# Performance work log

Measured on AMD Instinct MI355X. Metric: run time of the kernel, lower is better.

The kernel has to match this reference:

```python
import jax, jax.numpy as jnp
import numpy as np

B, T, I, H, L = 64, 2048, 128, 128, 2  # batch, seq_len, input, hidden, layers


def setup_inputs() -> dict:
    key = jax.random.key(0)
    ks = jax.random.split(key, 6)
    w = lambda k, shape: jax.random.normal(k, shape, dtype=jnp.float32) * 0.05
    return {
        "x": jax.random.normal(ks[0], (B, T, I), dtype=jnp.float32),
        "Wx0": w(ks[1], (4 * H, I)),
        "Wh0": w(ks[2], (4 * H, H)),
        "b0": jnp.zeros((4 * H,), jnp.float32),
        "Wx1": w(ks[3], (4 * H, H)),
        "Wh1": w(ks[4], (4 * H, H)),
        "b1": jnp.zeros((4 * H,), jnp.float32),
    }


def _cell(x_t, h, c, Wx, Wh, b):
    # fused-gate GEMM; gate order (i, f, g, o) matches the torch cell exactly
    gates = x_t @ Wx.T + h @ Wh.T + b  # [B, 4H]
    i, f, g, o = jnp.split(gates, 4, axis=-1)
    i = jax.nn.sigmoid(i)
    f = jax.nn.sigmoid(f)
    g = jnp.tanh(g)
    o = jax.nn.sigmoid(o)
    c_new = f * c + i * g
    h_new = o * jnp.tanh(c_new)
    return h_new, c_new


def reference(x, Wx0, Wh0, b0, Wx1, Wh1, b1):
    params = [(Wx0, Wh0, b0), (Wx1, Wh1, b1)]
    bsz = x.shape[0]
    hidden = Wh0.shape[1]
    h0 = jnp.zeros((L, bsz, hidden), x.dtype)
    c0 = jnp.zeros((L, bsz, hidden), x.dtype)

    def step(carry, x_t):
        h, c = carry
        hs, cs = [], []
        inp = x_t
        for l, (Wx, Wh, b) in enumerate(params):  # fixed, tiny layer loop
            hl, cl = _cell(inp, h[l], c[l], Wx, Wh, b)
            inp = hl
            hs.append(hl)
            cs.append(cl)
        return (jnp.stack(hs), jnp.stack(cs)), inp

    (hT, cT), ys = jax.lax.scan(step, (h0, c0), jnp.swapaxes(x, 0, 1))
    output = jnp.swapaxes(ys, 0, 1)  # [B, T, H], top-layer hidden states
    return output, hT, cT
```

## Files before the change

kernel.cpp:

```cpp
#include <hip/hip_runtime.h>
#include <hip/hip_fp16.h>

#define BB 64
#define TT 2048
#define II 128
#define HH 128
#define NG 512
#define CH 128
#define NCH (TT / CH)

typedef _Float16 h2_t __attribute__((ext_vector_type(2)));

#if defined(__has_builtin)
#if __has_builtin(__builtin_amdgcn_fdot2)
#define HAVE_FDOT2 1
#endif
#endif

__device__ __forceinline__ float fdot2f(h2_t a, h2_t b, float c) {
#ifdef HAVE_FDOT2
  return __builtin_amdgcn_fdot2(a, b, c, false);
#else
  return c + (float)a[0] * (float)b[0] + (float)a[1] * (float)b[1];
#endif
}

__device__ __forceinline__ float fast_sigmoid(float x) {
  float t = __builtin_amdgcn_exp2f(-1.4426950408889634f * x);
  return __builtin_amdgcn_rcpf(1.0f + t);
}
__device__ __forceinline__ float act_gate(float x, bool tanh_sel) {
  float xx = tanh_sel ? 2.0f * x : x;
  float s = fast_sigmoid(xx);
  return tanh_sel ? 2.0f * s - 1.0f : s;
}
__device__ __forceinline__ float fast_tanh(float x) {
  return 2.0f * fast_sigmoid(2.0f * x) - 1.0f;
}

__device__ __forceinline__ float dpp_xor1(float x) {
  return __int_as_float(__builtin_amdgcn_update_dpp(0, __float_as_int(x), 0xB1, 0xF, 0xF, true));
}
__device__ __forceinline__ float dpp_xor2(float x) {
  return __int_as_float(__builtin_amdgcn_update_dpp(0, __float_as_int(x), 0x4E, 0xF, 0xF, true));
}

__device__ __forceinline__ void bar_lds() {
  __builtin_amdgcn_fence(__ATOMIC_RELEASE, "workgroup", "local");
  __builtin_amdgcn_s_barrier();
  __builtin_amdgcn_fence(__ATOMIC_ACQUIRE, "workgroup", "local");
}

union LD4 {
  float4 f4;
  h2_t h[4];
};
union LDB {
  uint4 u4;
  h2_t h[4];
};

__device__ __forceinline__ unsigned aload(unsigned* p) { return atomicAdd(p, 0u); }

__global__ void w_transpose(const float* __restrict__ W, float* __restrict__ WT) {
  int idx = blockIdx.x * 256 + threadIdx.x;
  if (idx < NG * II) {
    int n = idx >> 7;
    int k = idx & 127;
    WT[k * NG + n] = W[idx];
  }
}

__global__ __launch_bounds__(256) void xg_gemm(const float* __restrict__ X,
                                               const float* __restrict__ WT,
                                               const float* __restrict__ bias,
                                               __half* __restrict__ Xg) {
  __shared__ float As[64][132];
  __shared__ float Bs[128][64];
  const int m0 = blockIdx.x * 64;
  const int n0 = blockIdx.y * 64;
  const int tid = threadIdx.x;

  {
    const float4* xv = (const float4*)(X + (size_t)m0 * II);
#pragma unroll
    for (int r = 0; r < 8; ++r) {
      int f = tid + 256 * r;
      int m = f >> 5;
      int c4 = f & 31;
      float4 v = xv[m * 32 + c4];
      *(float4*)&As[m][c4 * 4] = v;
    }
  }
  {
#pragma unroll
    for (int r = 0; r < 8; ++r) {
      int f = tid + 256 * r;
      int k = f >> 4;
      int q = f & 15;
      float4 v = *(const float4*)(WT + (size_t)k * NG + n0 + q * 4);
      *(float4*)&Bs[k][q * 4] = v;
    }
  }
  __syncthreads();

  const int tx = tid & 15;
  const int ty = tid >> 4;
  float acc[4][4];
#pragma unroll
  for (int i = 0; i < 4; ++i)
#pragma unroll
    for (int j = 0; j < 4; ++j) acc[i][j] = 0.0f;

#pragma unroll 4
  for (int k = 0; k < 128; ++k) {
    float a0 = As[ty * 4 + 0][k];
    float a1 = As[ty * 4 + 1][k];
    float a2 = As[ty * 4 + 2][k];
    float a3 = As[ty * 4 + 3][k];
    float4 bv = *(const float4*)&Bs[k][tx * 4];
    acc[0][0] = fmaf(a0, bv.x, acc[0][0]);
    acc[0][1] = fmaf(a0, bv.y, acc[0][1]);
    acc[0][2] = fmaf(a0, bv.z, acc[0][2]);
    acc[0][3] = fmaf(a0, bv.w, acc[0][3]);
    acc[1][0] = fmaf(a1, bv.x, acc[1][0]);
    acc[1][1] = fmaf(a1, bv.y, acc[1][1]);
    acc[1][2] = fmaf(a1, bv.z, acc[1][2]);
    acc[1][3] = fmaf(a1, bv.w, acc[1][3]);
    acc[2][0] = fmaf(a2, bv.x, acc[2][0]);
    acc[2][1] = fmaf(a2, bv.y, acc[2][1]);
    acc[2][2] = fmaf(a2, bv.z, acc[2][2]);
    acc[2][3] = fmaf(a2, bv.w, acc[2][3]);
    acc[3][0] = fmaf(a3, bv.x, acc[3][0]);
    acc[3][1] = fmaf(a3, bv.y, acc[3][1]);
    acc[3][2] = fmaf(a3, bv.z, acc[3][2]);
    acc[3][3] = fmaf(a3, bv.w, acc[3][3]);
  }

  float4 bvec = *(const float4*)(bias + n0 + tx * 4);
#pragma unroll
  for (int i = 0; i < 4; ++i) {
    int m = m0 + ty * 4 + i;
    __half2* dst = (__half2*)(Xg + (size_t)m * NG + n0 + tx * 4);
    dst[0] = __halves2half2(__float2half(acc[i][0] + bvec.x),
                            __float2half(acc[i][1] + bvec.y));
    dst[1] = __halves2half2(__float2half(acc[i][2] + bvec.z),
                            __float2half(acc[i][3] + bvec.w));
  }
}


__device__ __forceinline__ void roleA(int b, int n, char* smem,
    const __half* Xg, const float* __restrict__ Wh0,
    float* __restrict__ out, __half* hstream, unsigned* flag0)
{
  const int j = n >> 2;
  const int p = n & 3;
  const bool tsel = (p == 2);

  h2_t wh[4][16];
#pragma unroll
  for (int g = 0; g < 4; ++g) {
    const float2* ph = (const float2*)(Wh0 + (size_t)(g * 128 + j) * HH + p * 32);
#pragma unroll
    for (int k = 0; k < 16; ++k) {
      float2 v = ph[k];
      wh[g][k][0] = (_Float16)v.x;
      wh[g][k][1] = (_Float16)v.y;
    }
  }

  _Float16(*hb)[HH] = (_Float16(*)[HH])smem;
  if (n < HH) {
    hb[0][n] = (_Float16)0.0f;
    hb[1][n] = (_Float16)0.0f;
  }
  float c = 0.0f, hv = 0.0f;
  __syncthreads();

  const __half* xs = Xg + (size_t)b * TT * NG + p * 128 + j;
  float* hT = out + (size_t)BB * TT * HH;
  float* cT = hT + 2 * BB * HH;
  __half* hsp = hstream + (size_t)b * TT * HH + j;

  __half xg_c = xs[0];

#pragma unroll 1
  for (int cc = 0; cc < NCH; ++cc) {
#pragma unroll 1
    for (int s = 0; s < CH; ++s) {
      const int i = cc * CH + s;
      const int ip = (i + 1 < TT) ? i + 1 : i;
      __half xg_n = xs[(size_t)ip * NG];

      const char* H = (const char*)hb[i & 1] + p * 64;
      float a0 = 0.f, a1 = 0.f, a2 = 0.f, a3 = 0.f;
#pragma unroll
      for (int q = 0; q < 4; ++q) {
        LD4 u;
        u.f4 = *(const float4*)(H + q * 16);
#pragma unroll
        for (int t = 0; t < 4; ++t) {
          const int m = q * 4 + t;
          a0 = fdot2f(wh[0][m], u.h[t], a0);
          a1 = fdot2f(wh[1][m], u.h[t], a1);
          a2 = fdot2f(wh[2][m], u.h[t], a2);
          a3 = fdot2f(wh[3][m], u.h[t], a3);
        }
      }
      float k01 = (p & 1) ? a1 : a0;
      float u01 = (p & 1) ? a0 : a1;
      float r01 = k01 + dpp_xor1(u01);
      float k23 = (p & 1) ? a3 : a2;
      float u23 = (p & 1) ? a2 : a3;
      float r23 = k23 + dpp_xor1(u23);
      float kA = (p & 2) ? r23 : r01;
      float uA = (p & 2) ? r01 : r23;
      float sL = kA + dpp_xor2(uA);
      float aL = act_gate(sL + __half2float(xg_c), tsel);
      float fg = dpp_xor1(aL);
      float gg = dpp_xor2(aL);
      float og = dpp_xor2(fg);
      if (p == 0) {
        c = fg * c + aL * gg;
        hv = og * fast_tanh(c);
        _Float16 hf = (_Float16)hv;
        hb[(i & 1) ^ 1][j] = hf;
        *(_Float16*)(hsp + (size_t)i * HH) = hf;
      }
      bar_lds();
      xg_c = xg_n;
    }
    __syncthreads();
    if (n == 0) {
      __builtin_amdgcn_fence(__ATOMIC_RELEASE, "agent");
      atomicExch(flag0 + b * NCH + cc, 1u);
    }
  }

  if (p == 0) {
    hT[b * HH + j] = hv;
    cT[b * HH + j] = c;
  }
}

__device__ __forceinline__ void roleC(int cidx, int n, char* smem,
    __half* Xg, const __half* hstream, const float* __restrict__ WT1,
    const float* __restrict__ b1, unsigned* flag0, unsigned* flagC)
{
  const int b = cidx >> 1;
  const int half = cidx & 1;
  h2_t(*As2)[68] = (h2_t(*)[68])smem;
  h2_t(*Bs2)[64] = (h2_t(*)[64])(smem + 64 * 68 * 4);

  const int ty = n >> 4;
  const int tx = n & 15;

#pragma unroll 1
  for (int cc = 0; cc < NCH; ++cc) {
    if (n == 0) {
      while (aload(flag0 + b * NCH + cc) < 1u) __builtin_amdgcn_s_sleep(1);
    }
    __syncthreads();
    __builtin_amdgcn_fence(__ATOMIC_ACQUIRE, "agent");

    const int t0 = cc * CH + half * 64;
    {
      const int m = n >> 3, seg = n & 7;
      const uint4* src = (const uint4*)(hstream + ((size_t)b * TT + t0 + m) * HH + seg * 16);
      uint4 v0 = src[0], v1 = src[1];
      *(uint4*)&As2[m][seg * 8] = v0;
      *(uint4*)&As2[m][seg * 8 + 4] = v1;
    }

#pragma unroll 1
    for (int nt = 0; nt < 8; ++nt) {
      __syncthreads();
      {
        const int kp = n >> 3, cg = n & 7;
        const float4* w0 = (const float4*)(WT1 + (size_t)(2 * kp) * NG + nt * 64 + cg * 8);
        const float4* w1 = (const float4*)(WT1 + (size_t)(2 * kp + 1) * NG + nt * 64 + cg * 8);
        float4 x0 = w0[0], x1 = w0[1];
        float4 y0 = w1[0], y1 = w1[1];
        h2_t r[8];
        r[0][0] = (_Float16)x0.x; r[0][1] = (_Float16)y0.x;
        r[1][0] = (_Float16)x0.y; r[1][1] = (_Float16)y0.y;
        r[2][0] = (_Float16)x0.z; r[2][1] = (_Float16)y0.z;
        r[3][0] = (_Float16)x0.w; r[3][1] = (_Float16)y0.w;
        r[4][0] = (_Float16)x1.x; r[4][1] = (_Float16)y1.x;
        r[5][0] = (_Float16)x1.y; r[5][1] = (_Float16)y1.y;
        r[6][0] = (_Float16)x1.z; r[6][1] = (_Float16)y1.z;
        r[7][0] = (_Float16)x1.w; r[7][1] = (_Float16)y1.w;
        *(uint4*)&Bs2[kp][cg * 8] = *(uint4*)&r[0];
        *(uint4*)&Bs2[kp][cg * 8 + 4] = *(uint4*)&r[4];
      }
      __syncthreads();

      float acc[2][4];
#pragma unroll
      for (int r = 0; r < 2; ++r)
#pragma unroll
        for (int q = 0; q < 4; ++q) acc[r][q] = 0.0f;

#pragma unroll 4
      for (int k4 = 0; k4 < 16; ++k4) {
        LDB ua0, ua1;
        ua0.u4 = *(const uint4*)&As2[ty * 2][k4 * 4];
        ua1.u4 = *(const uint4*)&As2[ty * 2 + 1][k4 * 4];
#pragma unroll
        for (int t = 0; t < 4; ++t) {
          LDB ub;
          ub.u4 = *(const uint4*)&Bs2[k4 * 4 + t][tx * 4];
          acc[0][0] = fdot2f(ua0.h[t], ub.h[0], acc[0][0]);
          acc[0][1] = fdot2f(ua0.h[t], ub.h[1], acc[0][1]);
          acc[0][2] = fdot2f(ua0.h[t], ub.h[2], acc[0][2]);
          acc[0][3] = fdot2f(ua0.h[t], ub.h[3], acc[0][3]);
          acc[1][0] = fdot2f(ua1.h[t], ub.h[0], acc[1][0]);
          acc[1][1] = fdot2f(ua1.h[t], ub.h[1], acc[1][1]);
          acc[1][2] = fdot2f(ua1.h[t], ub.h[2], acc[1][2]);
          acc[1][3] = fdot2f(ua1.h[t], ub.h[3], acc[1][3]);
        }
      }

      const int col = nt * 64 + tx * 4;
      float4 bv = *(const float4*)(b1 + col);
#pragma unroll
      for (int r = 0; r < 2; ++r) {
        __half2* d = (__half2*)(Xg + ((size_t)b * TT + t0 + ty * 2 + r) * NG + col);
        d[0] = __halves2half2(__float2half(acc[r][0] + bv.x),
                              __float2half(acc[r][1] + bv.y));
        d[1] = __halves2half2(__float2half(acc[r][2] + bv.z),
                              __float2half(acc[r][3] + bv.w));
      }
    }
    __syncthreads();
    if (n == 0) {
      __builtin_amdgcn_fence(__ATOMIC_RELEASE, "agent");
      atomicAdd(flagC + b * NCH + cc, 1u);
    }
  }
}

__device__ __forceinline__ void roleB(int b, int n, char* smem,
    const __half* Xg, const float* __restrict__ Wh1,
    float* __restrict__ out, unsigned* flagC)
{
  const int j = n >> 2;
  const int p = n & 3;
  const bool tsel = (p == 2);

  h2_t wh[4][16];
#pragma unroll
  for (int g = 0; g < 4; ++g) {
    const float2* ph = (const float2*)(Wh1 + (size_t)(g * 128 + j) * HH + p * 32);
#pragma unroll
    for (int k = 0; k < 16; ++k) {
      float2 v = ph[k];
      wh[g][k][0] = (_Float16)v.x;
      wh[g][k][1] = (_Float16)v.y;
    }
  }

  _Float16(*hb)[HH] = (_Float16(*)[HH])smem;
  if (n < HH) {
    hb[0][n] = (_Float16)0.0f;
    hb[1][n] = (_Float16)0.0f;
  }
  float c = 0.0f, hv = 0.0f;
  __syncthreads();

  const __half* xs = Xg + (size_t)b * TT * NG + p * 128 + j;
  float* outp = out + (size_t)b * TT * HH;
  float* hT = out + (size_t)BB * TT * HH;
  float* cT = hT + 2 * BB * HH;

#pragma unroll 1
  for (int cc = 0; cc < NCH; ++cc) {
    if (n == 0) {
      while (aload(flagC + b * NCH + cc) < 2u) __builtin_amdgcn_s_sleep(1);
    }
    __syncthreads();
    __builtin_amdgcn_fence(__ATOMIC_ACQUIRE, "agent");

    __half xg_c = xs[(size_t)(cc * CH) * NG];
#pragma unroll 1
    for (int s = 0; s < CH; ++s) {
      const int i = cc * CH + s;
      __half xg_n = (s + 1 < CH) ? xs[(size_t)(i + 1) * NG] : __float2half(0.0f);

      const char* H = (const char*)hb[i & 1] + p * 64;
      float a0 = 0.f, a1 = 0.f, a2 = 0.f, a3 = 0.f;
#pragma unroll
      for (int q = 0; q < 4; ++q) {
        LD4 u;
        u.f4 = *(const float4*)(H + q * 16);
#pragma unroll
        for (int t = 0; t < 4; ++t) {
          const int m = q * 4 + t;
          a0 = fdot2f(wh[0][m], u.h[t], a0);
          a1 = fdot2f(wh[1][m], u.h[t], a1);
          a2 = fdot2f(wh[2][m], u.h[t], a2);
          a3 = fdot2f(wh[3][m], u.h[t], a3);
        }
      }
      float k01 = (p & 1) ? a1 : a0;
      float u01 = (p & 1) ? a0 : a1;
      float r01 = k01 + dpp_xor1(u01);
      float k23 = (p & 1) ? a3 : a2;
      float u23 = (p & 1) ? a2 : a3;
      float r23 = k23 + dpp_xor1(u23);
      float kA = (p & 2) ? r23 : r01;
      float uA = (p & 2) ? r01 : r23;
      float sL = kA + dpp_xor2(uA);
      float aL = act_gate(sL + __half2float(xg_c), tsel);
      float fg = dpp_xor1(aL);
      float gg = dpp_xor2(aL);
      float og = dpp_xor2(fg);
      if (p == 0) {
        c = fg * c + aL * gg;
        hv = og * fast_tanh(c);
        hb[(i & 1) ^ 1][j] = (_Float16)hv;
        outp[(size_t)i * HH + j] = hv;
      }
      bar_lds();
      xg_c = xg_n;
    }
  }

  if (p == 0) {
    hT[BB * HH + b * HH + j] = hv;
    cT[BB * HH + b * HH + j] = c;
  }
}

__global__
__attribute__((amdgpu_flat_work_group_size(512, 512)))
void lstm_mega(__half* Xg,
               __half* hstream,
               const float* __restrict__ Wh0,
               const float* __restrict__ Wh1,
               const float* __restrict__ WT1,
               const float* __restrict__ b1,
               float* __restrict__ out,
               unsigned* flag0, unsigned* flagC)
{
  __shared__ __align__(16) char smem[64 * 68 * 4 + 64 * 64 * 4];
  const int bid = blockIdx.x;
  const int n = threadIdx.x;
  if (bid < BB) {
    roleA(bid, n, smem, Xg, Wh0, out, hstream, flag0);
  } else if (bid < BB + 2 * BB) {
    roleC(bid - BB, n, smem, Xg, hstream, WT1, b1, flag0, flagC);
  } else {
    roleB(bid - 3 * BB, n, smem, Xg, Wh1, out, flagC);
  }
}

extern "C" void kernel_launch(void* const* d_in, const int* in_sizes, int n_in,
                              void* d_out, int out_size, void* d_ws, size_t ws_size,
                              hipStream_t stream) {
  const float* x   = (const float*)d_in[0];
  const float* Wx0 = (const float*)d_in[1];
  const float* Wh0 = (const float*)d_in[2];
  const float* b0  = (const float*)d_in[3];
  const float* Wx1 = (const float*)d_in[4];
  const float* Wh1 = (const float*)d_in[5];
  const float* b1  = (const float*)d_in[6];
  float* out = (float*)d_out;

  char* base = (char*)d_ws;
  __half* Xg = (__half*)base;
  size_t off = (size_t)BB * TT * NG * sizeof(__half);
  __half* hstream = (__half*)(base + off);
  off += (size_t)BB * TT * HH * sizeof(__half);
  float* WT0 = (float*)(base + off);
  off += (size_t)II * NG * sizeof(float);
  float* WT1 = (float*)(base + off);
  off += (size_t)II * NG * sizeof(float);
  unsigned* flag0 = (unsigned*)(base + off);
  off += (size_t)BB * NCH * sizeof(unsigned);
  unsigned* flagC = (unsigned*)(base + off);

  hipMemsetAsync(flag0, 0, 2 * (size_t)BB * NCH * sizeof(unsigned), stream);
  const int tgrid = (NG * II + 255) / 256;
  w_transpose<<<tgrid, 256, 0, stream>>>(Wx0, WT0);
  w_transpose<<<tgrid, 256, 0, stream>>>(Wx1, WT1);
  xg_gemm<<<dim3((BB * TT) / 64, NG / 64), 256, 0, stream>>>(x, WT0, b0, Xg);
  lstm_mega<<<4 * BB, 512, 0, stream>>>(Xg, hstream, Wh0, Wh1, WT1, b1, out,
                                        flag0, flagC);
}
```

Measured before the change: 1.538 ms.

## Batch 16 sequences per recurrent block and compute gates with MFMA

The recurrent roles for both layers are merged into one templated routine. Each workgroup now processes 16 batch rows at once and computes the hidden-to-gate product with 16x16x32 f16 MFMA instructions instead of per-sequence fdot2 plus DPP reductions. This cuts recurrent blocks from 64 per layer to 4, with the roleC flags aggregated per group of 16 sequences. The two weight transposes are fused into a single launch. The trade-off is far fewer workgroups on the serial path, with a per-step dependency on MFMA latency and a barrier.

```diff
diff --git a/kernel.cpp b/kernel.cpp
--- a/kernel.cpp
+++ b/kernel.cpp
@@ -8,8 +8,11 @@
 #define NG 512
 #define CH 128
 #define NCH (TT / CH)
+#define NA 4
 
 typedef _Float16 h2_t __attribute__((ext_vector_type(2)));
+typedef _Float16 f16x8 __attribute__((ext_vector_type(8)));
+typedef float f32x4 __attribute__((ext_vector_type(4)));
 
 #if defined(__has_builtin)
 #if __has_builtin(__builtin_amdgcn_fdot2)
@@ -29,20 +32,8 @@
   float t = __builtin_amdgcn_exp2f(-1.4426950408889634f * x);
   return __builtin_amdgcn_rcpf(1.0f + t);
 }
-__device__ __forceinline__ float act_gate(float x, bool tanh_sel) {
-  float xx = tanh_sel ? 2.0f * x : x;
-  float s = fast_sigmoid(xx);
-  return tanh_sel ? 2.0f * s - 1.0f : s;
-}
 __device__ __forceinline__ float fast_tanh(float x) {
   return 2.0f * fast_sigmoid(2.0f * x) - 1.0f;
-}
-
-__device__ __forceinline__ float dpp_xor1(float x) {
-  return __int_as_float(__builtin_amdgcn_update_dpp(0, __float_as_int(x), 0xB1, 0xF, 0xF, true));
-}
-__device__ __forceinline__ float dpp_xor2(float x) {
-  return __int_as_float(__builtin_amdgcn_update_dpp(0, __float_as_int(x), 0x4E, 0xF, 0xF, true));
 }
 
 __device__ __forceinline__ void bar_lds() {
@@ -51,24 +42,34 @@
   __builtin_amdgcn_fence(__ATOMIC_ACQUIRE, "workgroup", "local");
 }
 
-union LD4 {
+union LDH {
   float4 f4;
-  h2_t h[4];
+  f16x8 h8;
 };
 union LDB {
   uint4 u4;
   h2_t h[4];
 };
+union XU {
+  uint2 u;
+  __half h[4];
+};
+union HP {
+  _Float16 f[4];
+  uint2 u;
+};
 
 __device__ __forceinline__ unsigned aload(unsigned* p) { return atomicAdd(p, 0u); }
 
-__global__ void w_transpose(const float* __restrict__ W, float* __restrict__ WT) {
-  int idx = blockIdx.x * 256 + threadIdx.x;
-  if (idx < NG * II) {
-    int n = idx >> 7;
-    int k = idx & 127;
-    WT[k * NG + n] = W[idx];
-  }
+__global__ void w_transpose2(const float* __restrict__ W0, float* __restrict__ T0,
+                             const float* __restrict__ W1, float* __restrict__ T1) {
+  int bid = blockIdx.x;
+  const float* W = (bid < 256) ? W0 : W1;
+  float* T = (bid < 256) ? T0 : T1;
+  int idx = (bid & 255) * 256 + threadIdx.x;
+  int n = idx >> 7;
+  int k = idx & 127;
+  T[k * NG + n] = W[idx];
 }
 
 __global__ __launch_bounds__(256) void xg_gemm(const float* __restrict__ X,
@@ -149,104 +150,135 @@
   }
 }
 
-
-__device__ __forceinline__ void roleA(int b, int n, char* smem,
-    const __half* Xg, const float* __restrict__ Wh0,
-    float* __restrict__ out, __half* hstream, unsigned* flag0)
+#define HROW 136
+#define HBUF (16 * HROW)
+
+template <int LAYER>
+__device__ __forceinline__ void role_rec(int g, int tid, char* smem,
+    const __half* __restrict__ Xg, const float* __restrict__ Wh,
+    float* __restrict__ out, __half* __restrict__ hstream,
+    unsigned* flag0, unsigned* flagCg)
 {
-  const int j = n >> 2;
-  const int p = n & 3;
-  const bool tsel = (p == 2);
-
-  h2_t wh[4][16];
-#pragma unroll
-  for (int g = 0; g < 4; ++g) {
-    const float2* ph = (const float2*)(Wh0 + (size_t)(g * 128 + j) * HH + p * 32);
-#pragma unroll
-    for (int k = 0; k < 16; ++k) {
-      float2 v = ph[k];
-      wh[g][k][0] = (_Float16)v.x;
-      wh[g][k][1] = (_Float16)v.y;
-    }
-  }
-
-  _Float16(*hb)[HH] = (_Float16(*)[HH])smem;
-  if (n < HH) {
-    hb[0][n] = (_Float16)0.0f;
-    hb[1][n] = (_Float16)0.0f;
-  }
-  float c = 0.0f, hv = 0.0f;
+  const int w = tid >> 6;
+  const int l = tid & 63;
+  const int lrow = l & 15;
+  const int lk = l >> 4;
+  const int u0 = 16 * w + lk * 4;
+  const int bg = 16 * g + lrow;
+
+  f16x8 wf[4][4];
+#pragma unroll
+  for (int r = 0; r < 4; ++r)
+#pragma unroll
+    for (int kt = 0; kt < 4; ++kt) {
+      const float4* s4 = (const float4*)(Wh + (size_t)(128 * r + 16 * w + lrow) * HH + 32 * kt + 8 * lk);
+      float4 v0 = s4[0], v1 = s4[1];
+      f16x8 f;
+      f[0] = (_Float16)v0.x; f[1] = (_Float16)v0.y; f[2] = (_Float16)v0.z; f[3] = (_Float16)v0.w;
+      f[4] = (_Float16)v1.x; f[5] = (_Float16)v1.y; f[6] = (_Float16)v1.z; f[7] = (_Float16)v1.w;
+      wf[r][kt] = f;
+    }
+
+  _Float16* hb = (_Float16*)smem;
+  for (int i = tid; i < 2 * HBUF; i += 512) hb[i] = (_Float16)0.0f;
+  float c[4] = {0.f, 0.f, 0.f, 0.f};
+  float hq[4] = {0.f, 0.f, 0.f, 0.f};
   __syncthreads();
 
-  const __half* xs = Xg + (size_t)b * TT * NG + p * 128 + j;
+  const __half* XgL = Xg + (size_t)bg * TT * NG + u0;
   float* hT = out + (size_t)BB * TT * HH;
   float* cT = hT + 2 * BB * HH;
-  __half* hsp = hstream + (size_t)b * TT * HH + j;
-
-  __half xg_c = xs[0];
+  float* outp = out + (size_t)bg * TT * HH + u0;
+  __half* hsp = hstream + (size_t)bg * TT * HH + u0;
+
+  char* hbc = (char*)smem;
+  const int rdoff = lrow * (HROW * 2) + lk * 16;
+  const int wroff = lrow * (HROW * 2) + u0 * 2;
+
+  XU xc[4];
+  if (LAYER == 0) {
+#pragma unroll
+    for (int r = 0; r < 4; ++r) xc[r].u = *(const uint2*)(XgL + r * 128);
+  }
 
 #pragma unroll 1
   for (int cc = 0; cc < NCH; ++cc) {
+    if (LAYER == 1) {
+      if (tid == 0) {
+        while (aload(flagCg + g * NCH + cc) < 32u) __builtin_amdgcn_s_sleep(1);
+      }
+      __syncthreads();
+      __builtin_amdgcn_fence(__ATOMIC_ACQUIRE, "agent");
+      const __half* xb = XgL + (size_t)(cc * CH) * NG;
+#pragma unroll
+      for (int r = 0; r < 4; ++r) xc[r].u = *(const uint2*)(xb + r * 128);
+    }
+
 #pragma unroll 1
     for (int s = 0; s < CH; ++s) {
-      const int i = cc * CH + s;
-      const int ip = (i + 1 < TT) ? i + 1 : i;
-      __half xg_n = xs[(size_t)ip * NG];
-
-      const char* H = (const char*)hb[i & 1] + p * 64;
-      float a0 = 0.f, a1 = 0.f, a2 = 0.f, a3 = 0.f;
+      const int t = cc * CH + s;
+
+      const char* hr = hbc + (t & 1) * (HBUF * 2) + rdoff;
+      f32x4 a0 = {0.f, 0.f, 0.f, 0.f};
+      f32x4 a1 = a0, a2 = a0, a3 = a0;
+#pragma unroll
+      for (int kt = 0; kt < 4; ++kt) {
+        LDH u;
+        u.f4 = *(const float4*)(hr + kt * 64);
+        a0 = __builtin_amdgcn_mfma_f32_16x16x32_f16(wf[0][kt], u.h8, a0, 0, 0, 0);
+        a1 = __builtin_amdgcn_mfma_f32_16x16x32_f16(wf[1][kt], u.h8, a1, 0, 0, 0);
+        a2 = __builtin_amdgcn_mfma_f32_16x16x32_f16(wf[2][kt], u.h8, a2, 0, 0, 0);
+        a3 = __builtin_amdgcn_mfma_f32_16x16x32_f16(wf[3][kt], u.h8, a3, 0, 0, 0);
+      }
+
+      XU xn[4];
+      const bool pf = (LAYER == 0) ? (t + 1 < TT) : (s + 1 < CH);
+      if (pf) {
+        const __half* xb = XgL + (size_t)(t + 1) * NG;
+#pragma unroll
+        for (int r = 0; r < 4; ++r) xn[r].u = *(const uint2*)(xb + r * 128);
+      }
+
+      HP hp;
 #pragma unroll
       for (int q = 0; q < 4; ++q) {
-        LD4 u;
-        u.f4 = *(const float4*)(H + q * 16);
-#pragma unroll
-        for (int t = 0; t < 4; ++t) {
-          const int m = q * 4 + t;
-          a0 = fdot2f(wh[0][m], u.h[t], a0);
-          a1 = fdot2f(wh[1][m], u.h[t], a1);
-          a2 = fdot2f(wh[2][m], u.h[t], a2);
-          a3 = fdot2f(wh[3][m], u.h[t], a3);
-        }
-      }
-      float k01 = (p & 1) ? a1 : a0;
-      float u01 = (p & 1) ? a0 : a1;
-      float r01 = k01 + dpp_xor1(u01);
-      float k23 = (p & 1) ? a3 : a2;
-      float u23 = (p & 1) ? a2 : a3;
-      float r23 = k23 + dpp_xor1(u23);
-      float kA = (p & 2) ? r23 : r01;
-      float uA = (p & 2) ? r01 : r23;
-      float sL = kA + dpp_xor2(uA);
-      float aL = act_gate(sL + __half2float(xg_c), tsel);
-      float fg = dpp_xor1(aL);
-      float gg = dpp_xor2(aL);
-      float og = dpp_xor2(fg);
-      if (p == 0) {
-        c = fg * c + aL * gg;
-        hv = og * fast_tanh(c);
-        _Float16 hf = (_Float16)hv;
-        hb[(i & 1) ^ 1][j] = hf;
-        *(_Float16*)(hsp + (size_t)i * HH) = hf;
+        float gi = fast_sigmoid(a0[q] + __half2float(xc[0].h[q]));
+        float gf = fast_sigmoid(a1[q] + __half2float(xc[1].h[q]));
+        float gg = fast_tanh(a2[q] + __half2float(xc[2].h[q]));
+        float go = fast_sigmoid(a3[q] + __half2float(xc[3].h[q]));
+        c[q] = gf * c[q] + gi * gg;
+        float h = go * fast_tanh(c[q]);
+        hq[q] = h;
+        hp.f[q] = (_Float16)h;
+      }
+      *(uint2*)(hbc + ((t & 1) ^ 1) * (HBUF * 2) + wroff) = hp.u;
+      if (LAYER == 0) {
+        *(uint2*)(hsp + (size_t)t * HH) = hp.u;
+      } else {
+        float4 o4 = {hq[0], hq[1], hq[2], hq[3]};
+        *(float4*)(outp + (size_t)t * HH) = o4;
       }
       bar_lds();
-      xg_c = xg_n;
-    }
-    __syncthreads();
-    if (n == 0) {
+#pragma unroll
+      for (int r = 0; r < 4; ++r) xc[r].u = xn[r].u;
+    }
+
+    if (LAYER == 0) {
+      __syncthreads();
       __builtin_amdgcn_fence(__ATOMIC_RELEASE, "agent");
-      atomicExch(flag0 + b * NCH + cc, 1u);
-    }
-  }
-
-  if (p == 0) {
-    hT[b * HH + j] = hv;
-    cT[b * HH + j] = c;
-  }
+      if (tid < 16) atomicExch(flag0 + (16 * g + tid) * NCH + cc, 1u);
+    }
+  }
+
+  float4 hv4 = {hq[0], hq[1], hq[2], hq[3]};
+  float4 cv4 = {c[0], c[1], c[2], c[3]};
+  *(float4*)(hT + (size_t)LAYER * BB * HH + (size_t)bg * HH + u0) = hv4;
+  *(float4*)(cT + (size_t)LAYER * BB * HH + (size_t)bg * HH + u0) = cv4;
 }
 
 __device__ __forceinline__ void roleC(int cidx, int n, char* smem,
     __half* Xg, const __half* hstream, const float* __restrict__ WT1,
-    const float* __restrict__ b1, unsigned* flag0, unsigned* flagC)
+    const float* __restrict__ b1, unsigned* flag0, unsigned* flagCg)
 {
   const int b = cidx >> 1;
   const int half = cidx & 1;
@@ -336,123 +368,30 @@
     __syncthreads();
     if (n == 0) {
       __builtin_amdgcn_fence(__ATOMIC_RELEASE, "agent");
-      atomicAdd(flagC + b * NCH + cc, 1u);
-    }
-  }
-}
-
-__device__ __forceinline__ void roleB(int b, int n, char* smem,
-    const __half* Xg, const float* __restrict__ Wh1,
-    float* __restrict__ out, unsigned* flagC)
-{
-  const int j = n >> 2;
-  const int p = n & 3;
-  const bool tsel = (p == 2);
-
-  h2_t wh[4][16];
-#pragma unroll
-  for (int g = 0; g < 4; ++g) {
-    const float2* ph = (const float2*)(Wh1 + (size_t)(g * 128 + j) * HH + p * 32);
-#pragma unroll
-    for (int k = 0; k < 16; ++k) {
-      float2 v = ph[k];
-      wh[g][k][0] = (_Float16)v.x;
-      wh[g][k][1] = (_Float16)v.y;
-    }
-  }
-
-  _Float16(*hb)[HH] = (_Float16(*)[HH])smem;
-  if (n < HH) {
-    hb[0][n] = (_Float16)0.0f;
-    hb[1][n] = (_Float16)0.0f;
-  }
-  float c = 0.0f, hv = 0.0f;
-  __syncthreads();
-
-  const __half* xs = Xg + (size_t)b * TT * NG + p * 128 + j;
-  float* outp = out + (size_t)b * TT * HH;
-  float* hT = out + (size_t)BB * TT * HH;
-  float* cT = hT + 2 * BB * HH;
-
-#pragma unroll 1
-  for (int cc = 0; cc < NCH; ++cc) {
-    if (n == 0) {
-      while (aload(flagC + b * NCH + cc) < 2u) __builtin_amdgcn_s_sleep(1);
-    }
-    __syncthreads();
-    __builtin_amdgcn_fence(__ATOMIC_ACQUIRE, "agent");
-
-    __half xg_c = xs[(size_t)(cc * CH) * NG];
-#pragma unroll 1
-    for (int s = 0; s < CH; ++s) {
-      const int i = cc * CH + s;
-      __half xg_n = (s + 1 < CH) ? xs[(size_t)(i + 1) * NG] : __float2half(0.0f);
-
-      const char* H = (const char*)hb[i & 1] + p * 64;
-      float a0 = 0.f, a1 = 0.f, a2 = 0.f, a3 = 0.f;
-#pragma unroll
-      for (int q = 0; q < 4; ++q) {
-        LD4 u;
-        u.f4 = *(const float4*)(H + q * 16);
-#pragma unroll
-        for (int t = 0; t < 4; ++t) {
-          const int m = q * 4 + t;
-          a0 = fdot2f(wh[0][m], u.h[t], a0);
-          a1 = fdot2f(wh[1][m], u.h[t], a1);
-          a2 = fdot2f(wh[2][m], u.h[t], a2);
-          a3 = fdot2f(wh[3][m], u.h[t], a3);
-        }
-      }
-      float k01 = (p & 1) ? a1 : a0;
-      float u01 = (p & 1) ? a0 : a1;
-      float r01 = k01 + dpp_xor1(u01);
-      float k23 = (p & 1) ? a3 : a2;
-      float u23 = (p & 1) ? a2 : a3;
-      float r23 = k23 + dpp_xor1(u23);
-      float kA = (p & 2) ? r23 : r01;
-      float uA = (p & 2) ? r01 : r23;
-      float sL = kA + dpp_xor2(uA);
-      float aL = act_gate(sL + __half2float(xg_c), tsel);
-      float fg = dpp_xor1(aL);
-      float gg = dpp_xor2(aL);
-      float og = dpp_xor2(fg);
-      if (p == 0) {
-        c = fg * c + aL * gg;
-        hv = og * fast_tanh(c);
-        hb[(i & 1) ^ 1][j] = (_Float16)hv;
-        outp[(size_t)i * HH + j] = hv;
-      }
-      bar_lds();
-      xg_c = xg_n;
-    }
-  }
-
-  if (p == 0) {
-    hT[BB * HH + b * HH + j] = hv;
-    cT[BB * HH + b * HH + j] = c;
+      atomicAdd(flagCg + (b >> 4) * NCH + cc, 1u);
+    }
   }
 }
 
 __global__
 __attribute__((amdgpu_flat_work_group_size(512, 512)))
-void lstm_mega(__half* Xg,
-               __half* hstream,
+void lstm_mega(__half* Xg, __half* hstream,
                const float* __restrict__ Wh0,
                const float* __restrict__ Wh1,
                const float* __restrict__ WT1,
                const float* __restrict__ b1,
                float* __restrict__ out,
-               unsigned* flag0, unsigned* flagC)
+               unsigned* flag0, unsigned* flagCg)
 {
   __shared__ __align__(16) char smem[64 * 68 * 4 + 64 * 64 * 4];
   const int bid = blockIdx.x;
-  const int n = threadIdx.x;
-  if (bid < BB) {
-    roleA(bid, n, smem, Xg, Wh0, out, hstream, flag0);
-  } else if (bid < BB + 2 * BB) {
-    roleC(bid - BB, n, smem, Xg, hstream, WT1, b1, flag0, flagC);
+  const int tid = threadIdx.x;
+  if (bid < NA) {
+    role_rec<0>(bid, tid, smem, Xg, Wh0, out, hstream, flag0, flagCg);
+  } else if (bid < NA + 2 * BB) {
+    roleC(bid - NA, tid, smem, Xg, hstream, WT1, b1, flag0, flagCg);
   } else {
-    roleB(bid - 3 * BB, n, smem, Xg, Wh1, out, flagC);
+    role_rec<1>(bid - NA - 2 * BB, tid, smem, Xg, Wh1, out, hstream, flag0, flagCg);
   }
 }
 
@@ -478,14 +417,11 @@
   float* WT1 = (float*)(base + off);
   off += (size_t)II * NG * sizeof(float);
   unsigned* flag0 = (unsigned*)(base + off);
-  off += (size_t)BB * NCH * sizeof(unsigned);
-  unsigned* flagC = (unsigned*)(base + off);
-
-  hipMemsetAsync(flag0, 0, 2 * (size_t)BB * NCH * sizeof(unsigned), stream);
-  const int tgrid = (NG * II + 255) / 256;
-  w_transpose<<<tgrid, 256, 0, stream>>>(Wx0, WT0);
-  w_transpose<<<tgrid, 256, 0, stream>>>(Wx1, WT1);
+  unsigned* flagCg = flag0 + BB * NCH;
+
+  hipMemsetAsync(flag0, 0, (size_t)(BB * NCH + NA * NCH) * sizeof(unsigned), stream);
+  w_transpose2<<<512, 256, 0, stream>>>(Wx0, WT0, Wx1, WT1);
   xg_gemm<<<dim3((BB * TT) / 64, NG / 64), 256, 0, stream>>>(x, WT0, b0, Xg);
-  lstm_mega<<<4 * BB, 512, 0, stream>>>(Xg, hstream, Wh0, Wh1, WT1, b1, out,
-                                        flag0, flagC);
-}
+  lstm_mega<<<NA + 2 * BB + NA, 512, 0, stream>>>(Xg, hstream, Wh0, Wh1, WT1,
+                                                  b1, out, flag0, flagCg);
+}
```

Result: slower. 4.347 ms (+182.7%).

## Overlap layer-0 input projection with recurrence inside the persistent kernel

Applied to the files above, without the earlier changes.

The separate xg_gemm now computes only the first two time chunks (256 steps) per batch. The remaining chunks of the layer-0 input projection are computed by the roleC blocks two chunks ahead, which signal readiness through a new flagX counter that roleA waits on. The two weight-transpose launches are merged into one. The fdot2 accumulation chains in the recurrent roles are split into two partial sums to shorten dependency latency. This hides most of the large upfront GEMM behind the serial recurrence, at the cost of more spin-wait synchronisation and extra work on the roleC blocks.

```diff
diff --git a/kernel.cpp b/kernel.cpp
--- a/kernel.cpp
+++ b/kernel.cpp
@@ -62,27 +62,30 @@
 
 __device__ __forceinline__ unsigned aload(unsigned* p) { return atomicAdd(p, 0u); }
 
-__global__ void w_transpose(const float* __restrict__ W, float* __restrict__ WT) {
-  int idx = blockIdx.x * 256 + threadIdx.x;
-  if (idx < NG * II) {
-    int n = idx >> 7;
-    int k = idx & 127;
-    WT[k * NG + n] = W[idx];
-  }
-}
-
-__global__ __launch_bounds__(256) void xg_gemm(const float* __restrict__ X,
-                                               const float* __restrict__ WT,
-                                               const float* __restrict__ bias,
-                                               __half* __restrict__ Xg) {
+__global__ void w_transpose2(const float* __restrict__ W0, float* __restrict__ T0,
+                             const float* __restrict__ W1, float* __restrict__ T1) {
+  int bid = blockIdx.x;
+  const float* W = (bid < 256) ? W0 : W1;
+  float* T = (bid < 256) ? T0 : T1;
+  int idx = (bid & 255) * 256 + threadIdx.x;
+  int n = idx >> 7;
+  int k = idx & 127;
+  T[k * NG + n] = W[idx];
+}
+
+__global__ __launch_bounds__(256) void xg_gemm_pro(const float* __restrict__ X,
+                                                   const float* __restrict__ WT,
+                                                   const float* __restrict__ bias,
+                                                   __half* __restrict__ Xg) {
   __shared__ float As[64][132];
   __shared__ float Bs[128][64];
-  const int m0 = blockIdx.x * 64;
+  const int bx = blockIdx.x;
+  const size_t m0 = (size_t)(bx >> 2) * TT + (bx & 3) * 64;
   const int n0 = blockIdx.y * 64;
   const int tid = threadIdx.x;
 
   {
-    const float4* xv = (const float4*)(X + (size_t)m0 * II);
+    const float4* xv = (const float4*)(X + m0 * II);
 #pragma unroll
     for (int r = 0; r < 8; ++r) {
       int f = tid + 256 * r;
@@ -140,8 +143,8 @@
   float4 bvec = *(const float4*)(bias + n0 + tx * 4);
 #pragma unroll
   for (int i = 0; i < 4; ++i) {
-    int m = m0 + ty * 4 + i;
-    __half2* dst = (__half2*)(Xg + (size_t)m * NG + n0 + tx * 4);
+    size_t m = m0 + ty * 4 + i;
+    __half2* dst = (__half2*)(Xg + m * NG + n0 + tx * 4);
     dst[0] = __halves2half2(__float2half(acc[i][0] + bvec.x),
                             __float2half(acc[i][1] + bvec.y));
     dst[1] = __halves2half2(__float2half(acc[i][2] + bvec.z),
@@ -152,7 +155,8 @@
 
 __device__ __forceinline__ void roleA(int b, int n, char* smem,
     const __half* Xg, const float* __restrict__ Wh0,
-    float* __restrict__ out, __half* hstream, unsigned* flag0)
+    float* __restrict__ out, __half* hstream,
+    unsigned* flag0, unsigned* flagX)
 {
   const int j = n >> 2;
   const int p = n & 3;
@@ -183,31 +187,49 @@
   float* cT = hT + 2 * BB * HH;
   __half* hsp = hstream + (size_t)b * TT * HH + j;
 
-  __half xg_c = xs[0];
-
 #pragma unroll 1
   for (int cc = 0; cc < NCH; ++cc) {
+    if (cc >= 2) {
+      if (n == 0) {
+        while (aload(flagX + b * NCH + cc) < 2u) __builtin_amdgcn_s_sleep(1);
+      }
+      __syncthreads();
+      __builtin_amdgcn_fence(__ATOMIC_ACQUIRE, "agent");
+    }
+    __half xg_c = xs[(size_t)(cc * CH) * NG];
+
 #pragma unroll 1
     for (int s = 0; s < CH; ++s) {
       const int i = cc * CH + s;
-      const int ip = (i + 1 < TT) ? i + 1 : i;
-      __half xg_n = xs[(size_t)ip * NG];
+      __half xg_n = (s + 1 < CH) ? xs[(size_t)(i + 1) * NG] : __float2half(0.0f);
 
       const char* H = (const char*)hb[i & 1] + p * 64;
-      float a0 = 0.f, a1 = 0.f, a2 = 0.f, a3 = 0.f;
+      float s0a = 0.f, s0b = 0.f, s1a = 0.f, s1b = 0.f;
+      float s2a = 0.f, s2b = 0.f, s3a = 0.f, s3b = 0.f;
 #pragma unroll
       for (int q = 0; q < 4; ++q) {
         LD4 u;
         u.f4 = *(const float4*)(H + q * 16);
-#pragma unroll
-        for (int t = 0; t < 4; ++t) {
-          const int m = q * 4 + t;
-          a0 = fdot2f(wh[0][m], u.h[t], a0);
-          a1 = fdot2f(wh[1][m], u.h[t], a1);
-          a2 = fdot2f(wh[2][m], u.h[t], a2);
-          a3 = fdot2f(wh[3][m], u.h[t], a3);
-        }
-      }
+        const int m = q * 4;
+        s0a = fdot2f(wh[0][m + 0], u.h[0], s0a);
+        s0b = fdot2f(wh[0][m + 2], u.h[2], s0b);
+        s1a = fdot2f(wh[1][m + 0], u.h[0], s1a);
+        s1b = fdot2f(wh[1][m + 2], u.h[2], s1b);
+        s2a = fdot2f(wh[2][m + 0], u.h[0], s2a);
+        s2b = fdot2f(wh[2][m + 2], u.h[2], s2b);
+        s3a = fdot2f(wh[3][m + 0], u.h[0], s3a);
+        s3b = fdot2f(wh[3][m + 2], u.h[2], s3b);
+        s0a = fdot2f(wh[0][m + 1], u.h[1], s0a);
+        s0b = fdot2f(wh[0][m + 3], u.h[3], s0b);
+        s1a = fdot2f(wh[1][m + 1], u.h[1], s1a);
+        s1b = fdot2f(wh[1][m + 3], u.h[3], s1b);
+        s2a = fdot2f(wh[2][m + 1], u.h[1], s2a);
+        s2b = fdot2f(wh[2][m + 3], u.h[3], s2b);
+        s3a = fdot2f(wh[3][m + 1], u.h[1], s3a);
+        s3b = fdot2f(wh[3][m + 3], u.h[3], s3b);
+      }
+      float a0 = s0a + s0b, a1 = s1a + s1b, a2 = s2a + s2b, a3 = s3a + s3b;
+
       float k01 = (p & 1) ? a1 : a0;
       float u01 = (p & 1) ? a0 : a1;
       float r01 = k01 + dpp_xor1(u01);
@@ -245,8 +267,10 @@
 }
 
 __device__ __forceinline__ void roleC(int cidx, int n, char* smem,
-    __half* Xg, const __half* hstream, const float* __restrict__ WT1,
-    const float* __restrict__ b1, unsigned* flag0, unsigned* flagC)
+    __half* Xg, const __half* hstream, const float* __restrict__ x,
+    const float* __restrict__ WT0, const float* __restrict__ b0,
+    const float* __restrict__ WT1, const float* __restrict__ b1,
+    unsigned* flag0, unsigned* flagC, unsigned* flagX)
 {
   const int b = cidx >> 1;
   const int half = cidx & 1;
@@ -255,9 +279,93 @@
 
   const int ty = n >> 4;
   const int tx = n & 15;
+  const int mf = n >> 3;
+  const int sf = n & 7;
 
 #pragma unroll 1
   for (int cc = 0; cc < NCH; ++cc) {
+    if (cc + 2 < NCH) {
+      const int t0x = (cc + 2) * CH + half * 64;
+      {
+        const float4* sx = (const float4*)(x + ((size_t)b * TT + t0x + mf) * II + sf * 16);
+        float4 p0 = sx[0], p1 = sx[1], p2 = sx[2], p3 = sx[3];
+        h2_t r[8];
+        r[0][0] = (_Float16)p0.x; r[0][1] = (_Float16)p0.y;
+        r[1][0] = (_Float16)p0.z; r[1][1] = (_Float16)p0.w;
+        r[2][0] = (_Float16)p1.x; r[2][1] = (_Float16)p1.y;
+        r[3][0] = (_Float16)p1.z; r[3][1] = (_Float16)p1.w;
+        r[4][0] = (_Float16)p2.x; r[4][1] = (_Float16)p2.y;
+        r[5][0] = (_Float16)p2.z; r[5][1] = (_Float16)p2.w;
+        r[6][0] = (_Float16)p3.x; r[6][1] = (_Float16)p3.y;
+        r[7][0] = (_Float16)p3.z; r[7][1] = (_Float16)p3.w;
+        *(uint4*)&As2[mf][sf * 8] = *(uint4*)&r[0];
+        *(uint4*)&As2[mf][sf * 8 + 4] = *(uint4*)&r[4];
+      }
+#pragma unroll 1
+      for (int nt = 0; nt < 8; ++nt) {
+        __syncthreads();
+        {
+          const int kp = n >> 3, cg = n & 7;
+          const float4* w0 = (const float4*)(WT0 + (size_t)(2 * kp) * NG + nt * 64 + cg * 8);
+          const float4* w1 = (const float4*)(WT0 + (size_t)(2 * kp + 1) * NG + nt * 64 + cg * 8);
+          float4 x0 = w0[0], x1 = w0[1];
+          float4 y0 = w1[0], y1 = w1[1];
+          h2_t r[8];
+          r[0][0] = (_Float16)x0.x; r[0][1] = (_Float16)y0.x;
+          r[1][0] = (_Float16)x0.y; r[1][1] = (_Float16)y0.y;
+          r[2][0] = (_Float16)x0.z; r[2][1] = (_Float16)y0.z;
+          r[3][0] = (_Float16)x0.w; r[3][1] = (_Float16)y0.w;
+          r[4][0] = (_Float16)x1.x; r[4][1] = (_Float16)y1.x;
+          r[5][0] = (_Float16)x1.y; r[5][1] = (_Float16)y1.y;
+          r[6][0] = (_Float16)x1.z; r[6][1] = (_Float16)y1.z;
+          r[7][0] = (_Float16)x1.w; r[7][1] = (_Float16)y1.w;
+          *(uint4*)&Bs2[kp][cg * 8] = *(uint4*)&r[0];
+          *(uint4*)&Bs2[kp][cg * 8 + 4] = *(uint4*)&r[4];
+        }
+        __syncthreads();
+
+        float acc[2][4];
+#pragma unroll
+        for (int r = 0; r < 2; ++r)
+#pragma unroll
+          for (int q = 0; q < 4; ++q) acc[r][q] = 0.0f;
+#pragma unroll 4
+        for (int k4 = 0; k4 < 16; ++k4) {
+          LDB ua0, ua1;
+          ua0.u4 = *(const uint4*)&As2[ty * 2][k4 * 4];
+          ua1.u4 = *(const uint4*)&As2[ty * 2 + 1][k4 * 4];
+#pragma unroll
+          for (int t = 0; t < 4; ++t) {
+            LDB ub;
+            ub.u4 = *(const uint4*)&Bs2[k4 * 4 + t][tx * 4];
+            acc[0][0] = fdot2f(ua0.h[t], ub.h[0], acc[0][0]);
+            acc[0][1] = fdot2f(ua0.h[t], ub.h[1], acc[0][1]);
+            acc[0][2] = fdot2f(ua0.h[t], ub.h[2], acc[0][2]);
+            acc[0][3] = fdot2f(ua0.h[t], ub.h[3], acc[0][3]);
+            acc[1][0] = fdot2f(ua1.h[t], ub.h[0], acc[1][0]);
+            acc[1][1] = fdot2f(ua1.h[t], ub.h[1], acc[1][1]);
+            acc[1][2] = fdot2f(ua1.h[t], ub.h[2], acc[1][2]);
+            acc[1][3] = fdot2f(ua1.h[t], ub.h[3], acc[1][3]);
+          }
+        }
+        const int col = nt * 64 + tx * 4;
+        float4 bv = *(const float4*)(b0 + col);
+#pragma unroll
+        for (int r = 0; r < 2; ++r) {
+          __half2* d = (__half2*)(Xg + ((size_t)b * TT + t0x + ty * 2 + r) * NG + col);
+          d[0] = __halves2half2(__float2half(acc[r][0] + bv.x),
+                                __float2half(acc[r][1] + bv.y));
+          d[1] = __halves2half2(__float2half(acc[r][2] + bv.z),
+                                __float2half(acc[r][3] + bv.w));
+        }
+      }
+      __syncthreads();
+      if (n == 0) {
+        __builtin_amdgcn_fence(__ATOMIC_RELEASE, "agent");
+        atomicAdd(flagX + b * NCH + cc + 2, 1u);
+      }
+    }
+
     if (n == 0) {
       while (aload(flag0 + b * NCH + cc) < 1u) __builtin_amdgcn_s_sleep(1);
     }
@@ -266,13 +374,11 @@
 
     const int t0 = cc * CH + half * 64;
     {
-      const int m = n >> 3, seg = n & 7;
-      const uint4* src = (const uint4*)(hstream + ((size_t)b * TT + t0 + m) * HH + seg * 16);
+      const uint4* src = (const uint4*)(hstream + ((size_t)b * TT + t0 + mf) * HH + sf * 16);
       uint4 v0 = src[0], v1 = src[1];
-      *(uint4*)&As2[m][seg * 8] = v0;
-      *(uint4*)&As2[m][seg * 8 + 4] = v1;
-    }
-
+      *(uint4*)&As2[mf][sf * 8] = v0;
+      *(uint4*)&As2[mf][sf * 8 + 4] = v1;
+    }
 #pragma unroll 1
     for (int nt = 0; nt < 8; ++nt) {
       __syncthreads();
@@ -301,7 +407,6 @@
       for (int r = 0; r < 2; ++r)
 #pragma unroll
         for (int q = 0; q < 4; ++q) acc[r][q] = 0.0f;
-
 #pragma unroll 4
       for (int k4 = 0; k4 < 16; ++k4) {
         LDB ua0, ua1;
@@ -321,7 +426,6 @@
           acc[1][3] = fdot2f(ua1.h[t], ub.h[3], acc[1][3]);
         }
       }
-
       const int col = nt * 64 + tx * 4;
       float4 bv = *(const float4*)(b1 + col);
 #pragma unroll
@@ -389,20 +493,32 @@
       __half xg_n = (s + 1 < CH) ? xs[(size_t)(i + 1) * NG] : __float2half(0.0f);
 
       const char* H = (const char*)hb[i & 1] + p * 64;
-      float a0 = 0.f, a1 = 0.f, a2 = 0.f, a3 = 0.f;
+      float s0a = 0.f, s0b = 0.f, s1a = 0.f, s1b = 0.f;
+      float s2a = 0.f, s2b = 0.f, s3a = 0.f, s3b = 0.f;
 #pragma unroll
       for (int q = 0; q < 4; ++q) {
         LD4 u;
         u.f4 = *(const float4*)(H + q * 16);
-#pragma unroll
-        for (int t = 0; t < 4; ++t) {
-          const int m = q * 4 + t;
-          a0 = fdot2f(wh[0][m], u.h[t], a0);
-          a1 = fdot2f(wh[1][m], u.h[t], a1);
-          a2 = fdot2f(wh[2][m], u.h[t], a2);
-          a3 = fdot2f(wh[3][m], u.h[t], a3);
-        }
-      }
+        const int m = q * 4;
+        s0a = fdot2f(wh[0][m + 0], u.h[0], s0a);
+        s0b = fdot2f(wh[0][m + 2], u.h[2], s0b);
+        s1a = fdot2f(wh[1][m + 0], u.h[0], s1a);
+        s1b = fdot2f(wh[1][m + 2], u.h[2], s1b);
+        s2a = fdot2f(wh[2][m + 0], u.h[0], s2a);
+        s2b = fdot2f(wh[2][m + 2], u.h[2], s2b);
+        s3a = fdot2f(wh[3][m + 0], u.h[0], s3a);
+        s3b = fdot2f(wh[3][m + 2], u.h[2], s3b);
+        s0a = fdot2f(wh[0][m + 1], u.h[1], s0a);
+        s0b = fdot2f(wh[0][m + 3], u.h[3], s0b);
+        s1a = fdot2f(wh[1][m + 1], u.h[1], s1a);
+        s1b = fdot2f(wh[1][m + 3], u.h[3], s1b);
+        s2a = fdot2f(wh[2][m + 1], u.h[1], s2a);
+        s2b = fdot2f(wh[2][m + 3], u.h[3], s2b);
+        s3a = fdot2f(wh[3][m + 1], u.h[1], s3a);
+        s3b = fdot2f(wh[3][m + 3], u.h[3], s3b);
+      }
+      float a0 = s0a + s0b, a1 = s1a + s1b, a2 = s2a + s2b, a3 = s3a + s3b;
+
       float k01 = (p & 1) ? a1 : a0;
       float u01 = (p & 1) ? a0 : a1;
       float r01 = k01 + dpp_xor1(u01);
@@ -435,22 +551,24 @@
 
 __global__
 __attribute__((amdgpu_flat_work_group_size(512, 512)))
-void lstm_mega(__half* Xg,
-               __half* hstream,
+void lstm_mega(__half* Xg, __half* hstream, const float* __restrict__ x,
                const float* __restrict__ Wh0,
                const float* __restrict__ Wh1,
+               const float* __restrict__ WT0,
+               const float* __restrict__ b0,
                const float* __restrict__ WT1,
                const float* __restrict__ b1,
                float* __restrict__ out,
-               unsigned* flag0, unsigned* flagC)
+               unsigned* flag0, unsigned* flagC, unsigned* flagX)
 {
   __shared__ __align__(16) char smem[64 * 68 * 4 + 64 * 64 * 4];
   const int bid = blockIdx.x;
   const int n = threadIdx.x;
   if (bid < BB) {
-    roleA(bid, n, smem, Xg, Wh0, out, hstream, flag0);
+    roleA(bid, n, smem, Xg, Wh0, out, hstream, flag0, flagX);
   } else if (bid < BB + 2 * BB) {
-    roleC(bid - BB, n, smem, Xg, hstream, WT1, b1, flag0, flagC);
+    roleC(bid - BB, n, smem, Xg, hstream, x, WT0, b0, WT1, b1,
+          flag0, flagC, flagX);
   } else {
     roleB(bid - 3 * BB, n, smem, Xg, Wh1, out, flagC);
   }
@@ -478,14 +596,12 @@
   float* WT1 = (float*)(base + off);
   off += (size_t)II * NG * sizeof(float);
   unsigned* flag0 = (unsigned*)(base + off);
-  off += (size_t)BB * NCH * sizeof(unsigned);
-  unsigned* flagC = (unsigned*)(base + off);
-
-  hipMemsetAsync(flag0, 0, 2 * (size_t)BB * NCH * sizeof(unsigned), stream);
-  const int tgrid = (NG * II + 255) / 256;
-  w_transpose<<<tgrid, 256, 0, stream>>>(Wx0, WT0);
-  w_transpose<<<tgrid, 256, 0, stream>>>(Wx1, WT1);
-  xg_gemm<<<dim3((BB * TT) / 64, NG / 64), 256, 0, stream>>>(x, WT0, b0, Xg);
-  lstm_mega<<<4 * BB, 512, 0, stream>>>(Xg, hstream, Wh0, Wh1, WT1, b1, out,
-                                        flag0, flagC);
-}
+  unsigned* flagC = flag0 + BB * NCH;
+  unsigned* flagX = flagC + BB * NCH;
+
+  hipMemsetAsync(flag0, 0, 3 * (size_t)BB * NCH * sizeof(unsigned), stream);
+  w_transpose2<<<512, 256, 0, stream>>>(Wx0, WT0, Wx1, WT1);
+  xg_gemm_pro<<<dim3(BB * 4, NG / 64), 256, 0, stream>>>(x, WT0, b0, Xg);
+  lstm_mega<<<4 * BB, 512, 0, stream>>>(Xg, hstream, x, Wh0, Wh1, WT0, b0,
+                                        WT1, b1, out, flag0, flagC, flagX);
+}
```

Result: faster. 1.433 ms (-6.8%).
